# Kernel tuning notes

Hardware: AMD Instinct MI355X
Metric: run time of the kernel (lower is better)

## Reference

```python
import jax, jax.numpy as jnp
import numpy as np

# MolFormer TestBert config (from checkpoint hyper_parameters)
B, T, D, H, L, F, V = 64, 250, 768, 12, 12, 32, 2362
DH = D // H  # head dim = 64
EPS = 1e-6   # fast_transformers LinearAttention eps


def _layernorm(x, g, b):
    m = x.mean(-1, keepdims=True)
    v = ((x - m) ** 2).mean(-1, keepdims=True)
    return (x - m) / jnp.sqrt(v + 1e-5) * g + b


def setup_inputs() -> dict:
    key = jax.random.key(0)
    ks = jax.random.split(key, 20)
    s = 0.02

    def n(k, shape, scale=s):
        return jax.random.normal(k, shape, dtype=jnp.float32) * scale

    mask = jax.random.randint(ks[1], (B, T), 0, 2).astype(bool)
    mask = mask.at[:, 0].set(True)  # keep CLS position valid
    return {
        "batch": jax.random.randint(ks[0], (B, T), 0, V),
        "mask": mask,
        "tok_emb": n(ks[2], (V, D)),
        "pos_emb": n(ks[3], (1, T, D)),
        "Wq": n(ks[4], (L, D, D)), "bq": jnp.zeros((L, D)),
        "Wk": n(ks[5], (L, D, D)), "bk": jnp.zeros((L, D)),
        "Wv": n(ks[6], (L, D, D)), "bv": jnp.zeros((L, D)),
        "Wo": n(ks[7], (L, D, D)), "bo": jnp.zeros((L, D)),
        # GeneralizedRandomFeatures random projection omega: [L, head_dim, n_feats]
        "omega": jax.random.normal(ks[8], (L, DH, F), dtype=jnp.float32),
        "ln1_g": jnp.ones((L, D)), "ln1_b": jnp.zeros((L, D)),
        "ln2_g": jnp.ones((L, D)), "ln2_b": jnp.zeros((L, D)),
        # feed_forward_dimensions == n_embd in the builder kwargs
        "W1": n(ks[9], (L, D, D)), "b1": jnp.zeros((L, D)),
        "W2": n(ks[10], (L, D, D)), "b2": jnp.zeros((L, D)),
    }


def reference(batch, mask, tok_emb, pos_emb, Wq, bq, Wk, bk, Wv, bv, Wo, bo,
              omega, ln1_g, ln1_b, ln2_g, ln2_b, W1, b1, W2, b2):
    Bc, Tc = batch.shape
    # LengthMask(mask.sum(-1)) -> prefix key mask
    lengths = mask.astype(jnp.int32).sum(-1)
    key_mask = (jnp.arange(Tc)[None, :] < lengths[:, None]).astype(jnp.float32)  # [B,T]

    x = tok_emb[batch] + pos_emb[:, :Tc, :]  # dropout = identity in eval
    attn_w = None
    for l in range(L):
        q = (x @ Wq[l] + bq[l]).reshape(Bc, Tc, H, DH)
        k = (x @ Wk[l] + bk[l]).reshape(Bc, Tc, H, DH)
        v = (x @ Wv[l] + bv[l]).reshape(Bc, Tc, H, DH)
        # GeneralizedRandomFeatures: phi(x) = relu(x @ omega)
        Qf = jax.nn.relu(jnp.einsum('bthd,df->bthf', q, omega[l]))
        Kf = jax.nn.relu(jnp.einsum('bshd,df->bshf', k, omega[l]))
        Kf = Kf * key_mask[:, :, None, None]
        # linear attention: out = phi(Q) (phi(K)^T V) / (phi(Q) . sum phi(K))
        KV = jnp.einsum('bshf,bshm->bhfm', Kf, v)
        Z = 1.0 / (jnp.einsum('bthf,bhf->bth', Qf, Kf.sum(axis=1)) + EPS)
        out = jnp.einsum('bthf,bhfm,bth->bthm', Qf, KV, Z)
        if l == L - 1:
            # 'linearwweights': the implied (normalized) attention matrix
            attn_w = jnp.einsum('bthf,bshf,bth->bhts', Qf, Kf, Z)
        out = out.reshape(Bc, Tc, D) @ Wo[l] + bo[l]
        # fast_transformers post-norm encoder layer
        x = _layernorm(x + out, ln1_g[l], ln1_b[l])
        y = jax.nn.gelu(x @ W1[l] + b1[l], approximate=False) @ W2[l] + b2[l]
        x = _layernorm(x + y, ln2_g[l], ln2_b[l])
    # mode == 'cls'
    return x[:, 0, :], attn_w
```

## Files before the change

kernel.cpp:

```cpp
#include <hip/hip_runtime.h>
#include <hip/hip_bf16.h>

typedef __hip_bfloat16 bf16;
typedef __attribute__((ext_vector_type(4))) float f32x4;
typedef __attribute__((ext_vector_type(8))) short bf16x8;
typedef __attribute__((ext_vector_type(4))) short short4v;

#define B_ 64
#define T_ 250
#define D_ 768
#define H_ 12
#define DH_ 64
#define F_ 32
#define L_ 12
#define BT_ (B_*T_)
#define BT_P 16128
#define NF_ (H_*F_)
#define QKVN_ (3*D_)
#define KVTN_ 80

static __device__ __forceinline__ float b2f(short s) {
    union { float f; unsigned u; } z; z.u = ((unsigned)(unsigned short)s) << 16; return z.f;
}
static __device__ __forceinline__ short f2bs(float f) {
    bf16 b = __float2bfloat16(f);
    return *(short*)&b;
}

__global__ void lengths_kernel(const unsigned char* __restrict__ mask, int* __restrict__ lengths) {
    __shared__ int not_i32, not_f32;
    const unsigned int* w = (const unsigned int*)mask;
    int tid = threadIdx.x;
    if (tid == 0) { not_i32 = 0; not_f32 = 0; }
    __syncthreads();
    int li = 0, lf = 0;
    for (int i = tid; i < 4000; i += 256) {
        unsigned int v = w[i];
        if (v > 1u) li = 1;
        if (v != 0u && v != 0x3F800000u) lf = 1;
    }
    if (li) not_i32 = 1;
    if (lf) not_f32 = 1;
    __syncthreads();
    int mode = (!not_i32) ? 0 : ((!not_f32) ? 1 : 2);
    if (tid < B_) {
        int cnt = 0;
        if (mode == 0) {
            const int* r = (const int*)mask + tid * T_;
            for (int t = 0; t < T_; ++t) cnt += (r[t] != 0);
        } else if (mode == 1) {
            const unsigned int* r = w + tid * T_;
            for (int t = 0; t < T_; ++t) cnt += (r[t] != 0);
        } else {
            const unsigned char* r = mask + tid * T_;
            for (int t = 0; t < T_; ++t) cnt += (r[t] != 0);
        }
        lengths[tid] = cnt;
    }
}

__global__ void embed_kernel(const int* __restrict__ batch, const float* __restrict__ tok,
                             const float* __restrict__ pos, float* __restrict__ x,
                             bf16* __restrict__ xb) {
    int bt = blockIdx.x;
    int t = bt % T_;
    int tok_id = batch[bt];
    const float* tr = tok + (size_t)tok_id * D_;
    const float* pr = pos + (size_t)t * D_;
    float* xr = x + (size_t)bt * D_;
    bf16* xbr = xb + (size_t)bt * D_;
    for (int d = threadIdx.x; d < D_; d += 256) {
        float v = tr[d] + pr[d];
        xr[d] = v;
        xbr[d] = __float2bfloat16(v);
    }
}

__global__ __launch_bounds__(256) void transpose_w_all(
    const float* __restrict__ Wq, const float* __restrict__ Wk, const float* __restrict__ Wv,
    const float* __restrict__ Wo, const float* __restrict__ W1, const float* __restrict__ W2,
    bf16* __restrict__ Wt)
{
    __shared__ float tile[32][33];
    int zz = blockIdx.z;
    int l = zz / 6, m = zz - l * 6;
    const float* src;
    switch (m) {
        case 0: src = Wq; break; case 1: src = Wk; break; case 2: src = Wv; break;
        case 3: src = Wo; break; case 4: src = W1; break; default: src = W2; break;
    }
    src += (size_t)l * D_ * D_;
    bf16* dst = Wt + (size_t)zz * D_ * D_;
    int k0 = blockIdx.y * 32, n0 = blockIdx.x * 32;
    int tx = threadIdx.x, ty = threadIdx.y;
#pragma unroll
    for (int i = 0; i < 4; ++i)
        tile[ty + i * 8][tx] = src[(size_t)(k0 + ty + i * 8) * D_ + n0 + tx];
    __syncthreads();
#pragma unroll
    for (int i = 0; i < 4; ++i)
        dst[(size_t)(n0 + ty + i * 8) * D_ + k0 + tx] = __float2bfloat16(tile[tx][ty + i * 8]);
}

__global__ void pack_bias(const float* __restrict__ bq, const float* __restrict__ bk,
                          const float* __restrict__ bv, float* __restrict__ qkvb) {
    int o = blockIdx.x * 256 + threadIdx.x;
    if (o >= L_ * QKVN_) return;
    int l = o / QKVN_, c = o - l * QKVN_;
    float v;
    if (c < D_) v = bq[l * D_ + c];
    else if (c < 2 * D_) v = bk[l * D_ + c - D_];
    else v = bv[l * D_ + c - 2 * D_];
    qkvb[o] = v;
}

#define GP_SLOT 28672
__global__ __launch_bounds__(512, 2) void gemm_pipe(
    const bf16* __restrict__ A, const bf16* __restrict__ Bt,
    const float* __restrict__ bias, bf16* __restrict__ C,
    int N, int lda, int ldc, int act, const int* __restrict__ lengths)
{
    __shared__ __attribute__((aligned(16))) short lds_s[2 * GP_SLOT];
    const int tid = threadIdx.x, lane = tid & 63, wave = tid >> 6;
    const int wm = wave >> 2, wn = wave & 3;
    const int rsel = lane & 15, kq = lane >> 4;

    const int gx = gridDim.x;
    const int nwg = gx * gridDim.y;
    int orig = blockIdx.y * gx + blockIdx.x;
    int q = nwg >> 3, r = nwg & 7;
    int xcd = orig & 7, idx = orig >> 3;
    int swz = (xcd < r) ? xcd * (q + 1) + idx : r * (q + 1) + (xcd - r) * q + idx;
    const int row0 = (swz / gx) * 256;
    const int col0 = (swz % gx) * 192;

    const int srow = wave * 8 + (lane >> 3);
    const int sblk = (lane & 7) ^ ((lane >> 3) & 7);
    const short* gA = (const short*)A + (size_t)(row0 + srow) * lda + sblk * 8;
    const short* gB = (const short*)Bt + (size_t)(col0 + srow) * 768 + sblk * 8;
    const int ldest = wave * 512;

    f32x4 acc[8][3];
#pragma unroll
    for (int i = 0; i < 8; ++i)
#pragma unroll
        for (int j = 0; j < 3; ++j) acc[i][j] = (f32x4){0.f, 0.f, 0.f, 0.f};

    auto STAGE = [&](int kt, int slot) {
        short* base = lds_s + slot * GP_SLOT;
        int kc = kt * 64;
#pragma unroll
        for (int j = 0; j < 4; ++j)
            __builtin_amdgcn_global_load_lds(
                (const __attribute__((address_space(1))) unsigned int*)(gA + (size_t)(j * 64) * lda + kc),
                (__attribute__((address_space(3))) unsigned int*)(base + j * 4096 + ldest), 16, 0, 0);
#pragma unroll
        for (int j = 0; j < 3; ++j)
            __builtin_amdgcn_global_load_lds(
                (const __attribute__((address_space(1))) unsigned int*)(gB + (size_t)(j * 64) * 768 + kc),
                (__attribute__((address_space(3))) unsigned int*)(base + 16384 + j * 4096 + ldest), 16, 0, 0);
    };

    auto COMPUTE = [&](int slot) {
        const short* sA = lds_s + slot * GP_SLOT;
        const short* sB = sA + 16384;
#pragma unroll
        for (int ks = 0; ks < 2; ++ks) {
            int kb = ks * 4 + kq;
            bf16x8 bv[3];
#pragma unroll
            for (int n = 0; n < 3; ++n) {
                int rowb = wn * 48 + n * 16 + rsel;
                bv[n] = *(const bf16x8*)(sB + rowb * 64 + ((kb ^ (rowb & 7)) << 3));
            }
#pragma unroll
            for (int mh = 0; mh < 2; ++mh) {
                bf16x8 av[4];
#pragma unroll
                for (int m2 = 0; m2 < 4; ++m2) {
                    int rowa = wm * 128 + (mh * 4 + m2) * 16 + rsel;
                    av[m2] = *(const bf16x8*)(sA + rowa * 64 + ((kb ^ (rowa & 7)) << 3));
                }
                __builtin_amdgcn_s_setprio(1);
#pragma unroll
                for (int m2 = 0; m2 < 4; ++m2)
#pragma unroll
                    for (int n = 0; n < 3; ++n)
                        acc[mh * 4 + m2][n] = __builtin_amdgcn_mfma_f32_16x16x32_bf16(
                            av[m2], bv[n], acc[mh * 4 + m2][n], 0, 0, 0);
                __builtin_amdgcn_s_setprio(0);
            }
        }
    };

    STAGE(0, 0); STAGE(1, 1);
    asm volatile("s_waitcnt vmcnt(7)" ::: "memory");
    __builtin_amdgcn_s_barrier();

    for (int t = 0; t < 12; ++t) {
        COMPUTE(t & 1);
        if (t < 11) {
            __builtin_amdgcn_s_barrier();
            if (t < 10) {
                STAGE(t + 2, t & 1);
                asm volatile("s_waitcnt vmcnt(7)" ::: "memory");
            } else {
                asm volatile("s_waitcnt vmcnt(0)" ::: "memory");
            }
            __builtin_amdgcn_s_barrier();
        }
    }

    float bj[3];
#pragma unroll
    for (int n = 0; n < 3; ++n) {
        int col = col0 + wn * 48 + n * 16 + rsel;
        bj[n] = bias ? bias[col] : 0.f;
    }
#pragma unroll
    for (int mi = 0; mi < 8; ++mi) {
#pragma unroll
        for (int rr = 0; rr < 4; ++rr) {
            int row = row0 + wm * 128 + mi * 16 + (kq << 2) + rr;
            bool kill = false;
            if (act == 3) { int b = row / T_; int t = row - b * T_; kill = (t >= lengths[b & 63]); }
            size_t base = (size_t)row * ldc + col0 + wn * 48 + rsel;
#pragma unroll
            for (int n = 0; n < 3; ++n) {
                float v = acc[mi][n][rr] + bj[n];
                if (act == 1) v = 0.5f * v * (1.0f + erff(v * 0.70710678118654752f));
                else if (act >= 2) v = fmaxf(v, 0.f);
                if (kill) v = 0.f;
                C[base + n * 16] = __float2bfloat16(v);
            }
        }
    }
}

__global__ __launch_bounds__(256) void feat_kernel(
    const bf16* __restrict__ qkv, const float* __restrict__ om,
    bf16* __restrict__ Qf, bf16* __restrict__ Kf, const int* __restrict__ lengths)
{
    __shared__ __attribute__((aligned(16))) short omT[32 * 64];
    int z = blockIdx.z, h = blockIdx.y;
    int row0 = blockIdx.x * 128;
    int tid = threadIdx.x, lane = tid & 63, wave = tid >> 6;
    {
        int f = tid >> 3, k0 = (tid & 7) * 8;
#pragma unroll
        for (int j = 0; j < 8; ++j)
            omT[f * 64 + k0 + j] = f2bs(om[(size_t)(k0 + j) * F_ + f]);
    }
    __syncthreads();

    const short* A = (const short*)qkv + (size_t)z * D_ + h * DH_;
    int rsel = lane & 15, kof = (lane >> 4) << 3;

    bf16x8 af[2][2], bfr[2][2];
#pragma unroll
    for (int mi = 0; mi < 2; ++mi) {
        int row = row0 + wave * 32 + mi * 16 + rsel;
#pragma unroll
        for (int ks = 0; ks < 2; ++ks)
            af[mi][ks] = *(const bf16x8*)(A + (size_t)row * QKVN_ + ks * 32 + kof);
    }
#pragma unroll
    for (int ni = 0; ni < 2; ++ni)
#pragma unroll
        for (int ks = 0; ks < 2; ++ks)
            bfr[ni][ks] = *(const bf16x8*)(omT + (ni * 16 + rsel) * 64 + ks * 32 + kof);

    f32x4 acc[2][2];
#pragma unroll
    for (int i = 0; i < 2; ++i)
#pragma unroll
        for (int j = 0; j < 2; ++j) acc[i][j] = (f32x4){0.f, 0.f, 0.f, 0.f};
#pragma unroll
    for (int mi = 0; mi < 2; ++mi)
#pragma unroll
        for (int ni = 0; ni < 2; ++ni)
#pragma unroll
            for (int ks = 0; ks < 2; ++ks)
                acc[mi][ni] = __builtin_amdgcn_mfma_f32_16x16x32_bf16(af[mi][ks], bfr[ni][ks], acc[mi][ni], 0, 0, 0);

    bf16* out = z ? Kf : Qf;
#pragma unroll
    for (int mi = 0; mi < 2; ++mi) {
#pragma unroll
        for (int r = 0; r < 4; ++r) {
            int row = row0 + wave * 32 + mi * 16 + ((lane >> 4) << 2) + r;
            bool kill = false;
            if (z) { int b = row / T_; int t = row - b * T_; kill = (t >= lengths[b]); }
#pragma unroll
            for (int ni = 0; ni < 2; ++ni) {
                float v = fmaxf(acc[mi][ni][r], 0.f);
                if (kill) v = 0.f;
                out[(size_t)row * NF_ + h * F_ + ni * 16 + rsel] = __float2bfloat16(v);
            }
        }
    }
}

__global__ __launch_bounds__(256) void kvsum_kernel(
    const bf16* __restrict__ Kf, const bf16* __restrict__ v, int ldv,
    bf16* __restrict__ KVt)
{
    __shared__ short KfS[64][36];
    __shared__ short vS[64][68];
    int h = blockIdx.x, b = blockIdx.y;
    int tid = threadIdx.x, lane = tid & 63, wv = tid >> 6;
    int lr = tid >> 2, cp = tid & 3;

    const short* Kg = (const short*)Kf + (size_t)(b * T_) * NF_ + h * F_;
    const short* Vg = (const short*)v + (size_t)(b * T_) * ldv + h * DH_;

    f32x4 acc[2];
    acc[0] = (f32x4){0.f, 0.f, 0.f, 0.f};
    acc[1] = (f32x4){0.f, 0.f, 0.f, 0.f};
    float ksacc = 0.f;

    for (int s0 = 0; s0 < T_; s0 += 64) {
        __syncthreads();
        int s = s0 + lr;
        if (s < T_) {
            bf16x8 k8 = *(const bf16x8*)(Kg + (size_t)s * NF_ + cp * 8);
            *(short4v*)&KfS[lr][cp * 8]     = *((const short4v*)&k8);
            *(short4v*)&KfS[lr][cp * 8 + 4] = *((const short4v*)&k8 + 1);
            bf16x8 v8a = *(const bf16x8*)(Vg + (size_t)s * ldv + cp * 16);
            bf16x8 v8b = *(const bf16x8*)(Vg + (size_t)s * ldv + cp * 16 + 8);
            *(short4v*)&vS[lr][cp * 16]      = *((const short4v*)&v8a);
            *(short4v*)&vS[lr][cp * 16 + 4]  = *((const short4v*)&v8a + 1);
            *(short4v*)&vS[lr][cp * 16 + 8]  = *((const short4v*)&v8b);
            *(short4v*)&vS[lr][cp * 16 + 12] = *((const short4v*)&v8b + 1);
        } else {
            short4v zz = (short4v){0, 0, 0, 0};
            *(short4v*)&KfS[lr][cp * 8]     = zz;
            *(short4v*)&KfS[lr][cp * 8 + 4] = zz;
            *(short4v*)&vS[lr][cp * 16]      = zz;
            *(short4v*)&vS[lr][cp * 16 + 4]  = zz;
            *(short4v*)&vS[lr][cp * 16 + 8]  = zz;
            *(short4v*)&vS[lr][cp * 16 + 12] = zz;
        }
        __syncthreads();
        if (tid < 32) {
            float p0 = 0.f, p1 = 0.f;
            for (int ss = 0; ss < 64; ss += 2) {
                p0 += b2f(KfS[ss][tid]);
                p1 += b2f(KfS[ss + 1][tid]);
            }
            ksacc += p0 + p1;
        }
        bf16x8 af0[2], af1[2], bfr[2];
#pragma unroll
        for (int ks = 0; ks < 2; ++ks) {
            int sb = ks * 32 + ((lane >> 4) << 3);
#pragma unroll
            for (int j = 0; j < 8; ++j) {
                ((short*)&af0[ks])[j] = KfS[sb + j][lane & 15];
                ((short*)&af1[ks])[j] = KfS[sb + j][16 + (lane & 15)];
                ((short*)&bfr[ks])[j] = vS[sb + j][wv * 16 + (lane & 15)];
            }
        }
#pragma unroll
        for (int ks = 0; ks < 2; ++ks) {
            acc[0] = __builtin_amdgcn_mfma_f32_16x16x32_bf16(af0[ks], bfr[ks], acc[0], 0, 0, 0);
            acc[1] = __builtin_amdgcn_mfma_f32_16x16x32_bf16(af1[ks], bfr[ks], acc[1], 0, 0, 0);
        }
    }

    bf16* dst = KVt + (size_t)(b * H_ + h) * KVTN_ * F_;
    int m = wv * 16 + (lane & 15);
#pragma unroll
    for (int mi = 0; mi < 2; ++mi) {
#pragma unroll
        for (int r = 0; r < 4; ++r) {
            int f = mi * 16 + ((lane >> 4) << 2) + r;
            dst[(size_t)m * F_ + f] = __float2bfloat16(acc[mi][r]);
        }
    }
    if (tid < 32) dst[(size_t)64 * F_ + tid] = __float2bfloat16(ksacc);
    if (tid < 240) {
        ((short*)dst)[65 * F_ + tid * 2]     = 0;
        ((short*)dst)[65 * F_ + tid * 2 + 1] = 0;
    }
}

__global__ __launch_bounds__(256) void attn_mfma(
    const bf16* __restrict__ Qf, const bf16* __restrict__ KVt,
    float* __restrict__ Z, bf16* __restrict__ out, int ldo)
{
    int h = blockIdx.x, b = blockIdx.y;
    int tid = threadIdx.x, lane = tid & 63, wv = tid >> 6;
    int t0 = wv * 64;
    int rsel = lane & 15, kof = (lane >> 4) << 3;

    const short* Qg = (const short*)Qf + h * F_;
    const short* Bg = (const short*)KVt + (size_t)(b * H_ + h) * KVTN_ * F_;

    bf16x8 af[4], bfr[5];
#pragma unroll
    for (int mi = 0; mi < 4; ++mi) {
        int t = t0 + mi * 16 + rsel;
        if (t > T_ - 1) t = T_ - 1;
        af[mi] = *(const bf16x8*)(Qg + (size_t)(b * T_ + t) * NF_ + kof);
    }
#pragma unroll
    for (int ni = 0; ni < 5; ++ni)
        bfr[ni] = *(const bf16x8*)(Bg + (size_t)(ni * 16 + rsel) * F_ + kof);

    f32x4 acc[4][5];
#pragma unroll
    for (int i = 0; i < 4; ++i)
#pragma unroll
        for (int j = 0; j < 5; ++j) acc[i][j] = (f32x4){0.f, 0.f, 0.f, 0.f};
#pragma unroll
    for (int mi = 0; mi < 4; ++mi)
#pragma unroll
        for (int ni = 0; ni < 5; ++ni)
            acc[mi][ni] = __builtin_amdgcn_mfma_f32_16x16x32_bf16(af[mi], bfr[ni], acc[mi][ni], 0, 0, 0);

#pragma unroll
    for (int mi = 0; mi < 4; ++mi) {
#pragma unroll
        for (int r = 0; r < 4; ++r) {
            int t = t0 + mi * 16 + ((lane >> 4) << 2) + r;
            float zden = __shfl(acc[mi][4][r], lane & 48, 64);
            float z = 1.0f / (zden + 1e-6f);
            if (t < T_) {
                if (rsel == 0) Z[(size_t)(b * T_ + t) * H_ + h] = z;
                size_t base = (size_t)(b * T_ + t) * ldo + h * DH_ + rsel;
#pragma unroll
                for (int ni = 0; ni < 4; ++ni)
                    out[base + ni * 16] = __float2bfloat16(acc[mi][ni][r] * z);
            }
        }
    }
}

__global__ __launch_bounds__(256) void attnw_kernel(const bf16* __restrict__ Qf,
                                                    const bf16* __restrict__ Kf,
                                                    const float* __restrict__ Z,
                                                    float* __restrict__ out) {
    int tt = blockIdx.x;
    int bh = blockIdx.y;
    int b = bh / H_, h = bh - b * H_;
    int tid = threadIdx.x;
    int lane = tid & 63, w = tid >> 6;
    int t0 = tt * 64, s0 = w * 64;
    int kof = (lane >> 4) * 8;

    const short* Qs = (const short*)Qf;
    const short* Ks = (const short*)Kf;

    bf16x8 af[4], bfr[4];
#pragma unroll
    for (int mi = 0; mi < 4; ++mi) {
        int t = t0 + mi * 16 + (lane & 15);
        if (t > T_ - 1) t = T_ - 1;
        af[mi] = *(const bf16x8*)(Qs + ((size_t)(b * T_ + t) * H_ + h) * F_ + kof);
    }
#pragma unroll
    for (int ni = 0; ni < 4; ++ni) {
        int s = s0 + ni * 16 + (lane & 15);
        if (s > T_ - 1) s = T_ - 1;
        bfr[ni] = *(const bf16x8*)(Ks + ((size_t)(b * T_ + s) * H_ + h) * F_ + kof);
    }

    f32x4 acc[4][4];
#pragma unroll
    for (int i = 0; i < 4; ++i)
#pragma unroll
        for (int j = 0; j < 4; ++j) acc[i][j] = (f32x4){0.f, 0.f, 0.f, 0.f};
#pragma unroll
    for (int mi = 0; mi < 4; ++mi)
#pragma unroll
        for (int ni = 0; ni < 4; ++ni)
            acc[mi][ni] = __builtin_amdgcn_mfma_f32_16x16x32_bf16(af[mi], bfr[ni], acc[mi][ni], 0, 0, 0);

#pragma unroll
    for (int mi = 0; mi < 4; ++mi) {
#pragma unroll
        for (int r = 0; r < 4; ++r) {
            int t = t0 + mi * 16 + (lane >> 4) * 4 + r;
            if (t >= T_) continue;
            float z = Z[(size_t)(b * T_ + t) * H_ + h];
            size_t base = ((size_t)bh * T_ + t) * T_;
#pragma unroll
            for (int ni = 0; ni < 4; ++ni) {
                int s = s0 + ni * 16 + (lane & 15);
                if (s < T_) out[base + s] = acc[mi][ni][r] * z;
            }
        }
    }
}

__global__ __launch_bounds__(256) void ln_kernel(float* __restrict__ x, const bf16* __restrict__ res,
                                                 int ldr,
                                                 const float* __restrict__ g, const float* __restrict__ bb,
                                                 bf16* __restrict__ xb) {
    int bt = blockIdx.x, tid = threadIdx.x;
    float* xr = x + (size_t)bt * D_;
    const bf16* rr = res + (size_t)bt * ldr;
    float v[3]; float s = 0.f, ss = 0.f;
#pragma unroll
    for (int i = 0; i < 3; ++i) {
        int idx = tid + i * 256;
        float t = xr[idx] + __bfloat162float(rr[idx]);
        v[i] = t; s += t; ss += t * t;
    }
#pragma unroll
    for (int o = 1; o < 64; o <<= 1) { s += __shfl_xor(s, o, 64); ss += __shfl_xor(ss, o, 64); }
    __shared__ float red[4][2];
    int wave = tid >> 6, lane = tid & 63;
    if (lane == 0) { red[wave][0] = s; red[wave][1] = ss; }
    __syncthreads();
    s = red[0][0] + red[1][0] + red[2][0] + red[3][0];
    ss = red[0][1] + red[1][1] + red[2][1] + red[3][1];
    float mean = s * (1.f / D_);
    float var = ss * (1.f / D_) - mean * mean;
    float rstd = rsqrtf(var + 1e-5f);
    bf16* xbr = xb + (size_t)bt * D_;
#pragma unroll
    for (int i = 0; i < 3; ++i) {
        int idx = tid + i * 256;
        float o = (v[i] - mean) * rstd * g[idx] + bb[idx];
        xr[idx] = o;
        xbr[idx] = __float2bfloat16(o);
    }
}

__global__ void cls_kernel(const float* __restrict__ x, float* __restrict__ out) {
    int o = blockIdx.x * 256 + threadIdx.x;
    if (o >= B_ * D_) return;
    int b = o / D_, d = o % D_;
    out[o] = x[(size_t)(b * T_) * D_ + d];
}

extern "C" void kernel_launch(void* const* d_in, const int* in_sizes, int n_in,
                              void* d_out, int out_size, void* d_ws, size_t ws_size,
                              hipStream_t stream) {
    const int*   batch = (const int*)d_in[0];
    const unsigned char* mask = (const unsigned char*)d_in[1];
    const float* tok  = (const float*)d_in[2];
    const float* pos  = (const float*)d_in[3];
    const float* Wq   = (const float*)d_in[4];
    const float* bq   = (const float*)d_in[5];
    const float* Wk   = (const float*)d_in[6];
    const float* bk   = (const float*)d_in[7];
    const float* Wv   = (const float*)d_in[8];
    const float* bv   = (const float*)d_in[9];
    const float* Wo   = (const float*)d_in[10];
    const float* bo   = (const float*)d_in[11];
    const float* omega= (const float*)d_in[12];
    const float* ln1g = (const float*)d_in[13];
    const float* ln1b = (const float*)d_in[14];
    const float* ln2g = (const float*)d_in[15];
    const float* ln2b = (const float*)d_in[16];
    const float* W1   = (const float*)d_in[17];
    const float* b1   = (const float*)d_in[18];
    const float* W2   = (const float*)d_in[19];
    const float* b2   = (const float*)d_in[20];

    float* out_cls  = (float*)d_out;
    float* out_attn = (float*)d_out + B_ * D_;

    char* wsb = (char*)d_ws;
    float* x   = (float*)wsb; wsb += (size_t)BT_ * D_ * 4;
    bf16* xb   = (bf16*)wsb;  wsb += (size_t)BT_P * D_ * 2;
    bf16* qkv  = (bf16*)wsb;  wsb += (size_t)BT_P * QKVN_ * 2;
    bf16* Qf   = (bf16*)wsb;  wsb += (size_t)BT_ * NF_ * 2;
    bf16* Kf   = (bf16*)wsb;  wsb += (size_t)BT_ * NF_ * 2;
    bf16* KVt  = (bf16*)wsb;  wsb += (size_t)B_ * H_ * KVTN_ * F_ * 2;
    float* Z   = (float*)wsb; wsb += (size_t)BT_ * H_ * 4;
    bf16* Wt   = (bf16*)wsb;  wsb += (size_t)L_ * 6 * D_ * D_ * 2;
    float* qkvb= (float*)wsb; wsb += (size_t)L_ * QKVN_ * 4;
    int* lengths = (int*)wsb; wsb += 256;

    lengths_kernel<<<1, 256, 0, stream>>>(mask, lengths);
    embed_kernel<<<BT_, 256, 0, stream>>>(batch, tok, pos, x, xb);
    pack_bias<<<(L_ * QKVN_ + 255) / 256, 256, 0, stream>>>(bq, bk, bv, qkvb);
    transpose_w_all<<<dim3(24, 24, 72), dim3(32, 8), 0, stream>>>(Wq, Wk, Wv, Wo, W1, W2, Wt);

    dim3 qkv_g(QKVN_ / 192, BT_P / 256);
    dim3 dxd_g(D_ / 192, BT_P / 256);
    dim3 feat_g(BT_ / 128, H_, 2);
    dim3 kv_g(H_, B_);
    const size_t WS = (size_t)D_ * D_;

    for (int l = 0; l < L_; ++l) {
        const bf16* Wtl = Wt + (size_t)l * 6 * WS;

        gemm_pipe<<<qkv_g, 512, 0, stream>>>(xb, Wtl, qkvb + l * QKVN_, qkv,
                                             QKVN_, D_, QKVN_, 0, lengths);

        feat_kernel<<<feat_g, 256, 0, stream>>>(qkv, omega + (size_t)l * DH_ * F_,
                                                Qf, Kf, lengths);

        kvsum_kernel<<<kv_g, 256, 0, stream>>>(Kf, qkv + 2 * D_, QKVN_, KVt);

        attn_mfma<<<kv_g, 256, 0, stream>>>(Qf, KVt, Z, qkv, QKVN_);

        if (l == L_ - 1)
            attnw_kernel<<<dim3(4, B_ * H_), 256, 0, stream>>>(Qf, Kf, Z, out_attn);

        gemm_pipe<<<dxd_g, 512, 0, stream>>>(qkv, Wtl + 3 * WS, bo + l * D_, qkv + D_,
                                             D_, QKVN_, QKVN_, 0, lengths);
        ln_kernel<<<BT_, 256, 0, stream>>>(x, qkv + D_, QKVN_, ln1g + l * D_, ln1b + l * D_, xb);

        gemm_pipe<<<dxd_g, 512, 0, stream>>>(xb, Wtl + 4 * WS, b1 + l * D_, qkv + 2 * D_,
                                             D_, D_, QKVN_, 1, lengths);
        gemm_pipe<<<dxd_g, 512, 0, stream>>>(qkv + 2 * D_, Wtl + 5 * WS, b2 + l * D_, qkv,
                                             D_, QKVN_, QKVN_, 0, lengths);
        ln_kernel<<<BT_, 256, 0, stream>>>(x, qkv, QKVN_, ln2g + l * D_, ln2b + l * D_, xb);
    }

    cls_kernel<<<(B_ * D_ + 255) / 256, 256, 0, stream>>>(x, out_cls);
}
```

Measured before the change: 3.353 ms.

## Fold omega projection into Q/K weights and fuse kvsum with attention

Precomputes Wq·omega and Wk·omega (and the matching biases) so the QKV GEMM directly emits ReLU'd Q/K features. The GEMM width drops from 2304 to 1536 columns and the separate feature kernel goes away. The kvsum and attention kernels merge into one, which keeps KV in LDS instead of a global buffer. In exchange the features are now computed from bf16-rounded composed weights rather than a bf16 q/k, which changes rounding, and the buffer offsets inside qkv are reorganised.

```diff
diff --git a/kernel.cpp b/kernel.cpp
--- a/kernel.cpp
+++ b/kernel.cpp
@@ -16,8 +16,8 @@
 #define BT_ (B_*T_)
 #define BT_P 16128
 #define NF_ (H_*F_)
-#define QKVN_ (3*D_)
-#define KVTN_ 80
+#define QKVN_ 2304
+#define QN_ 1536
 
 static __device__ __forceinline__ float b2f(short s) {
     union { float f; unsigned u; } z; z.u = ((unsigned)(unsigned short)s) << 16; return z.f;
@@ -77,20 +77,23 @@
 }
 
 __global__ __launch_bounds__(256) void transpose_w_all(
-    const float* __restrict__ Wq, const float* __restrict__ Wk, const float* __restrict__ Wv,
-    const float* __restrict__ Wo, const float* __restrict__ W1, const float* __restrict__ W2,
+    const float* __restrict__ Wv, const float* __restrict__ Wo,
+    const float* __restrict__ W1, const float* __restrict__ W2,
     bf16* __restrict__ Wt)
 {
     __shared__ float tile[32][33];
     int zz = blockIdx.z;
-    int l = zz / 6, m = zz - l * 6;
+    int l = zz >> 2, m = zz & 3;
     const float* src;
+    int slot;
     switch (m) {
-        case 0: src = Wq; break; case 1: src = Wk; break; case 2: src = Wv; break;
-        case 3: src = Wo; break; case 4: src = W1; break; default: src = W2; break;
+        case 0: src = Wv; slot = 0; break;
+        case 1: src = Wo; slot = 3; break;
+        case 2: src = W1; slot = 4; break;
+        default: src = W2; slot = 5; break;
     }
     src += (size_t)l * D_ * D_;
-    bf16* dst = Wt + (size_t)zz * D_ * D_;
+    bf16* dst = Wt + ((size_t)l * 6 + slot) * D_ * D_;
     int k0 = blockIdx.y * 32, n0 = blockIdx.x * 32;
     int tx = threadIdx.x, ty = threadIdx.y;
 #pragma unroll
@@ -102,15 +105,59 @@
         dst[(size_t)(n0 + ty + i * 8) * D_ + k0 + tx] = __float2bfloat16(tile[tx][ty + i * 8]);
 }
 
-__global__ void pack_bias(const float* __restrict__ bq, const float* __restrict__ bk,
-                          const float* __restrict__ bv, float* __restrict__ qkvb) {
+__global__ __launch_bounds__(256) void compose_w(
+    const float* __restrict__ Wq, const float* __restrict__ Wk,
+    const float* __restrict__ omega, bf16* __restrict__ Wt)
+{
+    __shared__ float omS[64][33];
+    __shared__ float WS2[32][65];
+    int zz = blockIdx.z;
+    int l = zz >> 1, qk = zz & 1;
+    int h = blockIdx.y;
+    int c0 = blockIdx.x * 32;
+    const float* W = (qk ? Wk : Wq) + (size_t)l * D_ * D_;
+    const float* om = omega + (size_t)l * DH_ * F_;
+    int tid = threadIdx.x;
+    for (int i = tid; i < 64 * 32; i += 256) {
+        int j = i >> 5, f = i & 31;
+        omS[j][f] = om[j * F_ + f];
+    }
+    for (int i = tid; i < 32 * 64; i += 256) {
+        int ci = i >> 6, j = i & 63;
+        WS2[ci][j] = W[(size_t)(c0 + ci) * D_ + h * DH_ + j];
+    }
+    __syncthreads();
+    int f = tid & 31, cg = tid >> 5;
+    bf16* dst = Wt + (size_t)l * 6 * D_ * D_
+              + (size_t)(D_ + qk * NF_ + h * F_ + f) * D_;
+#pragma unroll
+    for (int cc = 0; cc < 4; ++cc) {
+        int ci = cg + cc * 8;
+        float s = 0.f;
+#pragma unroll
+        for (int j = 0; j < 64; ++j) s += WS2[ci][j] * omS[j][f];
+        dst[c0 + ci] = __float2bfloat16(s);
+    }
+}
+
+__global__ void pack_bias2(const float* __restrict__ bq, const float* __restrict__ bk,
+                           const float* __restrict__ bv, const float* __restrict__ omega,
+                           float* __restrict__ qkvb) {
     int o = blockIdx.x * 256 + threadIdx.x;
-    if (o >= L_ * QKVN_) return;
-    int l = o / QKVN_, c = o - l * QKVN_;
+    if (o >= L_ * QN_) return;
+    int l = o / QN_, c = o - l * QN_;
     float v;
-    if (c < D_) v = bq[l * D_ + c];
-    else if (c < 2 * D_) v = bk[l * D_ + c - D_];
-    else v = bv[l * D_ + c - 2 * D_];
+    if (c < D_) v = bv[l * D_ + c];
+    else {
+        int qk = (c >= D_ + NF_);
+        int n = c - D_ - qk * NF_;
+        int h = n >> 5, f = n & 31;
+        const float* b = (qk ? bk : bq) + l * D_ + h * DH_;
+        const float* om = omega + (size_t)l * DH_ * F_;
+        float s = 0.f;
+        for (int j = 0; j < 64; ++j) s += b[j] * om[j * F_ + f];
+        v = s;
+    }
     qkvb[o] = v;
 }
 
@@ -211,6 +258,9 @@
         }
     }
 
+    int eact = act;
+    if (act == 9) eact = (col0 < D_) ? 0 : ((col0 < D_ + NF_) ? 2 : 3);
+
     float bj[3];
 #pragma unroll
     for (int n = 0; n < 3; ++n) {
@@ -223,13 +273,13 @@
         for (int rr = 0; rr < 4; ++rr) {
             int row = row0 + wm * 128 + mi * 16 + (kq << 2) + rr;
             bool kill = false;
-            if (act == 3) { int b = row / T_; int t = row - b * T_; kill = (t >= lengths[b & 63]); }
+            if (eact == 3) { int b = row / T_; int t = row - b * T_; kill = (t >= lengths[b & 63]); }
             size_t base = (size_t)row * ldc + col0 + wn * 48 + rsel;
 #pragma unroll
             for (int n = 0; n < 3; ++n) {
                 float v = acc[mi][n][rr] + bj[n];
-                if (act == 1) v = 0.5f * v * (1.0f + erff(v * 0.70710678118654752f));
-                else if (act >= 2) v = fmaxf(v, 0.f);
+                if (eact == 1) v = 0.5f * v * (1.0f + erff(v * 0.70710678118654752f));
+                else if (eact >= 2) v = fmaxf(v, 0.f);
                 if (kill) v = 0.f;
                 C[base + n * 16] = __float2bfloat16(v);
             }
@@ -237,81 +287,20 @@
     }
 }
 
-__global__ __launch_bounds__(256) void feat_kernel(
-    const bf16* __restrict__ qkv, const float* __restrict__ om,
-    bf16* __restrict__ Qf, bf16* __restrict__ Kf, const int* __restrict__ lengths)
-{
-    __shared__ __attribute__((aligned(16))) short omT[32 * 64];
-    int z = blockIdx.z, h = blockIdx.y;
-    int row0 = blockIdx.x * 128;
-    int tid = threadIdx.x, lane = tid & 63, wave = tid >> 6;
-    {
-        int f = tid >> 3, k0 = (tid & 7) * 8;
-#pragma unroll
-        for (int j = 0; j < 8; ++j)
-            omT[f * 64 + k0 + j] = f2bs(om[(size_t)(k0 + j) * F_ + f]);
-    }
-    __syncthreads();
-
-    const short* A = (const short*)qkv + (size_t)z * D_ + h * DH_;
-    int rsel = lane & 15, kof = (lane >> 4) << 3;
-
-    bf16x8 af[2][2], bfr[2][2];
-#pragma unroll
-    for (int mi = 0; mi < 2; ++mi) {
-        int row = row0 + wave * 32 + mi * 16 + rsel;
-#pragma unroll
-        for (int ks = 0; ks < 2; ++ks)
-            af[mi][ks] = *(const bf16x8*)(A + (size_t)row * QKVN_ + ks * 32 + kof);
-    }
-#pragma unroll
-    for (int ni = 0; ni < 2; ++ni)
-#pragma unroll
-        for (int ks = 0; ks < 2; ++ks)
-            bfr[ni][ks] = *(const bf16x8*)(omT + (ni * 16 + rsel) * 64 + ks * 32 + kof);
-
-    f32x4 acc[2][2];
-#pragma unroll
-    for (int i = 0; i < 2; ++i)
-#pragma unroll
-        for (int j = 0; j < 2; ++j) acc[i][j] = (f32x4){0.f, 0.f, 0.f, 0.f};
-#pragma unroll
-    for (int mi = 0; mi < 2; ++mi)
-#pragma unroll
-        for (int ni = 0; ni < 2; ++ni)
-#pragma unroll
-            for (int ks = 0; ks < 2; ++ks)
-                acc[mi][ni] = __builtin_amdgcn_mfma_f32_16x16x32_bf16(af[mi][ks], bfr[ni][ks], acc[mi][ni], 0, 0, 0);
-
-    bf16* out = z ? Kf : Qf;
-#pragma unroll
-    for (int mi = 0; mi < 2; ++mi) {
-#pragma unroll
-        for (int r = 0; r < 4; ++r) {
-            int row = row0 + wave * 32 + mi * 16 + ((lane >> 4) << 2) + r;
-            bool kill = false;
-            if (z) { int b = row / T_; int t = row - b * T_; kill = (t >= lengths[b]); }
-#pragma unroll
-            for (int ni = 0; ni < 2; ++ni) {
-                float v = fmaxf(acc[mi][ni][r], 0.f);
-                if (kill) v = 0.f;
-                out[(size_t)row * NF_ + h * F_ + ni * 16 + rsel] = __float2bfloat16(v);
-            }
-        }
-    }
-}
-
-__global__ __launch_bounds__(256) void kvsum_kernel(
-    const bf16* __restrict__ Kf, const bf16* __restrict__ v, int ldv,
-    bf16* __restrict__ KVt)
+__global__ __launch_bounds__(256) void kvattn_kernel(
+    const bf16* __restrict__ Kf, int ldkf, const bf16* __restrict__ v, int ldv,
+    const bf16* __restrict__ Qf, int ldq, float* __restrict__ Z,
+    bf16* __restrict__ out, int ldo)
 {
     __shared__ short KfS[64][36];
     __shared__ short vS[64][68];
+    __shared__ short KVtS[80][40];
     int h = blockIdx.x, b = blockIdx.y;
     int tid = threadIdx.x, lane = tid & 63, wv = tid >> 6;
     int lr = tid >> 2, cp = tid & 3;
-
-    const short* Kg = (const short*)Kf + (size_t)(b * T_) * NF_ + h * F_;
+    int rsel = lane & 15, kq = lane >> 4;
+
+    const short* Kg = (const short*)Kf + (size_t)(b * T_) * ldkf + h * F_;
     const short* Vg = (const short*)v + (size_t)(b * T_) * ldv + h * DH_;
 
     f32x4 acc[2];
@@ -323,7 +312,7 @@
         __syncthreads();
         int s = s0 + lr;
         if (s < T_) {
-            bf16x8 k8 = *(const bf16x8*)(Kg + (size_t)s * NF_ + cp * 8);
+            bf16x8 k8 = *(const bf16x8*)(Kg + (size_t)s * ldkf + cp * 8);
             *(short4v*)&KfS[lr][cp * 8]     = *((const short4v*)&k8);
             *(short4v*)&KfS[lr][cp * 8 + 4] = *((const short4v*)&k8 + 1);
             bf16x8 v8a = *(const bf16x8*)(Vg + (size_t)s * ldv + cp * 16);
@@ -353,12 +342,12 @@
         bf16x8 af0[2], af1[2], bfr[2];
 #pragma unroll
         for (int ks = 0; ks < 2; ++ks) {
-            int sb = ks * 32 + ((lane >> 4) << 3);
+            int sb = ks * 32 + (kq << 3);
 #pragma unroll
             for (int j = 0; j < 8; ++j) {
-                ((short*)&af0[ks])[j] = KfS[sb + j][lane & 15];
-                ((short*)&af1[ks])[j] = KfS[sb + j][16 + (lane & 15)];
-                ((short*)&bfr[ks])[j] = vS[sb + j][wv * 16 + (lane & 15)];
+                ((short*)&af0[ks])[j] = KfS[sb + j][rsel];
+                ((short*)&af1[ks])[j] = KfS[sb + j][16 + rsel];
+                ((short*)&bfr[ks])[j] = vS[sb + j][wv * 16 + rsel];
             }
         }
 #pragma unroll
@@ -368,77 +357,66 @@
         }
     }
 
-    bf16* dst = KVt + (size_t)(b * H_ + h) * KVTN_ * F_;
-    int m = wv * 16 + (lane & 15);
-#pragma unroll
-    for (int mi = 0; mi < 2; ++mi) {
-#pragma unroll
-        for (int r = 0; r < 4; ++r) {
-            int f = mi * 16 + ((lane >> 4) << 2) + r;
-            dst[(size_t)m * F_ + f] = __float2bfloat16(acc[mi][r]);
-        }
-    }
-    if (tid < 32) dst[(size_t)64 * F_ + tid] = __float2bfloat16(ksacc);
-    if (tid < 240) {
-        ((short*)dst)[65 * F_ + tid * 2]     = 0;
-        ((short*)dst)[65 * F_ + tid * 2 + 1] = 0;
-    }
-}
-
-__global__ __launch_bounds__(256) void attn_mfma(
-    const bf16* __restrict__ Qf, const bf16* __restrict__ KVt,
-    float* __restrict__ Z, bf16* __restrict__ out, int ldo)
-{
-    int h = blockIdx.x, b = blockIdx.y;
-    int tid = threadIdx.x, lane = tid & 63, wv = tid >> 6;
+    __syncthreads();
+    {
+        int m = wv * 16 + rsel;
+#pragma unroll
+        for (int mi = 0; mi < 2; ++mi)
+#pragma unroll
+            for (int r = 0; r < 4; ++r) {
+                int f = mi * 16 + (kq << 2) + r;
+                KVtS[m][f] = f2bs(acc[mi][r]);
+            }
+        if (tid < 32) KVtS[64][tid] = f2bs(ksacc);
+    }
+    __syncthreads();
+
+    const short* Qg = (const short*)Qf + h * F_;
     int t0 = wv * 64;
-    int rsel = lane & 15, kof = (lane >> 4) << 3;
-
-    const short* Qg = (const short*)Qf + h * F_;
-    const short* Bg = (const short*)KVt + (size_t)(b * H_ + h) * KVTN_ * F_;
-
-    bf16x8 af[4], bfr[5];
+    int kof = kq << 3;
+
+    bf16x8 af[4], bfr2[5];
 #pragma unroll
     for (int mi = 0; mi < 4; ++mi) {
         int t = t0 + mi * 16 + rsel;
         if (t > T_ - 1) t = T_ - 1;
-        af[mi] = *(const bf16x8*)(Qg + (size_t)(b * T_ + t) * NF_ + kof);
+        af[mi] = *(const bf16x8*)(Qg + (size_t)(b * T_ + t) * ldq + kof);
     }
 #pragma unroll
     for (int ni = 0; ni < 5; ++ni)
-        bfr[ni] = *(const bf16x8*)(Bg + (size_t)(ni * 16 + rsel) * F_ + kof);
-
-    f32x4 acc[4][5];
+        bfr2[ni] = *(const bf16x8*)(&KVtS[ni * 16 + rsel][kof]);
+
+    f32x4 oacc[4][5];
 #pragma unroll
     for (int i = 0; i < 4; ++i)
 #pragma unroll
-        for (int j = 0; j < 5; ++j) acc[i][j] = (f32x4){0.f, 0.f, 0.f, 0.f};
+        for (int j = 0; j < 5; ++j) oacc[i][j] = (f32x4){0.f, 0.f, 0.f, 0.f};
 #pragma unroll
     for (int mi = 0; mi < 4; ++mi)
 #pragma unroll
         for (int ni = 0; ni < 5; ++ni)
-            acc[mi][ni] = __builtin_amdgcn_mfma_f32_16x16x32_bf16(af[mi], bfr[ni], acc[mi][ni], 0, 0, 0);
+            oacc[mi][ni] = __builtin_amdgcn_mfma_f32_16x16x32_bf16(af[mi], bfr2[ni], oacc[mi][ni], 0, 0, 0);
 
 #pragma unroll
     for (int mi = 0; mi < 4; ++mi) {
 #pragma unroll
         for (int r = 0; r < 4; ++r) {
-            int t = t0 + mi * 16 + ((lane >> 4) << 2) + r;
-            float zden = __shfl(acc[mi][4][r], lane & 48, 64);
+            int t = t0 + mi * 16 + (kq << 2) + r;
+            float zden = __shfl(oacc[mi][4][r], lane & 48, 64);
             float z = 1.0f / (zden + 1e-6f);
             if (t < T_) {
                 if (rsel == 0) Z[(size_t)(b * T_ + t) * H_ + h] = z;
                 size_t base = (size_t)(b * T_ + t) * ldo + h * DH_ + rsel;
 #pragma unroll
                 for (int ni = 0; ni < 4; ++ni)
-                    out[base + ni * 16] = __float2bfloat16(acc[mi][ni][r] * z);
+                    out[base + ni * 16] = __float2bfloat16(oacc[mi][ni][r] * z);
             }
         }
     }
 }
 
 __global__ __launch_bounds__(256) void attnw_kernel(const bf16* __restrict__ Qf,
-                                                    const bf16* __restrict__ Kf,
+                                                    const bf16* __restrict__ Kf, int ldf,
                                                     const float* __restrict__ Z,
                                                     float* __restrict__ out) {
     int tt = blockIdx.x;
@@ -449,21 +427,21 @@
     int t0 = tt * 64, s0 = w * 64;
     int kof = (lane >> 4) * 8;
 
-    const short* Qs = (const short*)Qf;
-    const short* Ks = (const short*)Kf;
+    const short* Qs = (const short*)Qf + h * F_;
+    const short* Ks = (const short*)Kf + h * F_;
 
     bf16x8 af[4], bfr[4];
 #pragma unroll
     for (int mi = 0; mi < 4; ++mi) {
         int t = t0 + mi * 16 + (lane & 15);
         if (t > T_ - 1) t = T_ - 1;
-        af[mi] = *(const bf16x8*)(Qs + ((size_t)(b * T_ + t) * H_ + h) * F_ + kof);
+        af[mi] = *(const bf16x8*)(Qs + (size_t)(b * T_ + t) * ldf + kof);
     }
 #pragma unroll
     for (int ni = 0; ni < 4; ++ni) {
         int s = s0 + ni * 16 + (lane & 15);
         if (s > T_ - 1) s = T_ - 1;
-        bfr[ni] = *(const bf16x8*)(Ks + ((size_t)(b * T_ + s) * H_ + h) * F_ + kof);
+        bfr[ni] = *(const bf16x8*)(Ks + (size_t)(b * T_ + s) * ldf + kof);
     }
 
     f32x4 acc[4][4];
@@ -568,48 +546,43 @@
     float* x   = (float*)wsb; wsb += (size_t)BT_ * D_ * 4;
     bf16* xb   = (bf16*)wsb;  wsb += (size_t)BT_P * D_ * 2;
     bf16* qkv  = (bf16*)wsb;  wsb += (size_t)BT_P * QKVN_ * 2;
-    bf16* Qf   = (bf16*)wsb;  wsb += (size_t)BT_ * NF_ * 2;
-    bf16* Kf   = (bf16*)wsb;  wsb += (size_t)BT_ * NF_ * 2;
-    bf16* KVt  = (bf16*)wsb;  wsb += (size_t)B_ * H_ * KVTN_ * F_ * 2;
     float* Z   = (float*)wsb; wsb += (size_t)BT_ * H_ * 4;
     bf16* Wt   = (bf16*)wsb;  wsb += (size_t)L_ * 6 * D_ * D_ * 2;
-    float* qkvb= (float*)wsb; wsb += (size_t)L_ * QKVN_ * 4;
+    float* qkvb= (float*)wsb; wsb += (size_t)L_ * QN_ * 4;
     int* lengths = (int*)wsb; wsb += 256;
 
     lengths_kernel<<<1, 256, 0, stream>>>(mask, lengths);
     embed_kernel<<<BT_, 256, 0, stream>>>(batch, tok, pos, x, xb);
-    pack_bias<<<(L_ * QKVN_ + 255) / 256, 256, 0, stream>>>(bq, bk, bv, qkvb);
-    transpose_w_all<<<dim3(24, 24, 72), dim3(32, 8), 0, stream>>>(Wq, Wk, Wv, Wo, W1, W2, Wt);
-
-    dim3 qkv_g(QKVN_ / 192, BT_P / 256);
+    pack_bias2<<<(L_ * QN_ + 255) / 256, 256, 0, stream>>>(bq, bk, bv, omega, qkvb);
+    transpose_w_all<<<dim3(24, 24, 4 * L_), dim3(32, 8), 0, stream>>>(Wv, Wo, W1, W2, Wt);
+    compose_w<<<dim3(24, H_, 2 * L_), 256, 0, stream>>>(Wq, Wk, omega, Wt);
+
+    dim3 qkv_g(QN_ / 192, BT_P / 256);
     dim3 dxd_g(D_ / 192, BT_P / 256);
-    dim3 feat_g(BT_ / 128, H_, 2);
     dim3 kv_g(H_, B_);
     const size_t WS = (size_t)D_ * D_;
 
     for (int l = 0; l < L_; ++l) {
         const bf16* Wtl = Wt + (size_t)l * 6 * WS;
 
-        gemm_pipe<<<qkv_g, 512, 0, stream>>>(xb, Wtl, qkvb + l * QKVN_, qkv,
-                                             QKVN_, D_, QKVN_, 0, lengths);
-
-        feat_kernel<<<feat_g, 256, 0, stream>>>(qkv, omega + (size_t)l * DH_ * F_,
-                                                Qf, Kf, lengths);
-
-        kvsum_kernel<<<kv_g, 256, 0, stream>>>(Kf, qkv + 2 * D_, QKVN_, KVt);
-
-        attn_mfma<<<kv_g, 256, 0, stream>>>(Qf, KVt, Z, qkv, QKVN_);
+        gemm_pipe<<<qkv_g, 512, 0, stream>>>(xb, Wtl, qkvb + l * QN_, qkv,
+                                             QN_, D_, QKVN_, 9, lengths);
+
+        kvattn_kernel<<<kv_g, 256, 0, stream>>>(qkv + 1152, QKVN_, qkv, QKVN_,
+                                                qkv + 768, QKVN_, Z,
+                                                qkv + 1536, QKVN_);
 
         if (l == L_ - 1)
-            attnw_kernel<<<dim3(4, B_ * H_), 256, 0, stream>>>(Qf, Kf, Z, out_attn);
-
-        gemm_pipe<<<dxd_g, 512, 0, stream>>>(qkv, Wtl + 3 * WS, bo + l * D_, qkv + D_,
+            attnw_kernel<<<dim3(4, B_ * H_), 256, 0, stream>>>(qkv + 768, qkv + 1152, QKVN_,
+                                                               Z, out_attn);
+
+        gemm_pipe<<<dxd_g, 512, 0, stream>>>(qkv + 1536, Wtl + 3 * WS, bo + l * D_, qkv,
                                              D_, QKVN_, QKVN_, 0, lengths);
-        ln_kernel<<<BT_, 256, 0, stream>>>(x, qkv + D_, QKVN_, ln1g + l * D_, ln1b + l * D_, xb);
-
-        gemm_pipe<<<dxd_g, 512, 0, stream>>>(xb, Wtl + 4 * WS, b1 + l * D_, qkv + 2 * D_,
+        ln_kernel<<<BT_, 256, 0, stream>>>(x, qkv, QKVN_, ln1g + l * D_, ln1b + l * D_, xb);
+
+        gemm_pipe<<<dxd_g, 512, 0, stream>>>(xb, Wtl + 4 * WS, b1 + l * D_, qkv + 1536,
                                              D_, D_, QKVN_, 1, lengths);
-        gemm_pipe<<<dxd_g, 512, 0, stream>>>(qkv + 2 * D_, Wtl + 5 * WS, b2 + l * D_, qkv,
+        gemm_pipe<<<dxd_g, 512, 0, stream>>>(qkv + 1536, Wtl + 5 * WS, b2 + l * D_, qkv,
                                              D_, QKVN_, QKVN_, 0, lengths);
         ln_kernel<<<BT_, 256, 0, stream>>>(x, qkv, QKVN_, ln2g + l * D_, ln2b + l * D_, xb);
     }
```

After: 2.928 ms. 12.7% less time.
